# Optimization experiments

Hardware: AMD Instinct MI355X
Metric: run time of the kernel (lower is better)

The kernel has to match this reference:

```python
import jax, jax.numpy as jnp
import numpy as np

B, S, D = 2, 1024, 512
G, H, QKD, VD = 8, 8, 64, 64
FFOUT = D

def setup_inputs() -> dict:
    key = jax.random.key(0)
    ks = jax.random.split(key, 7)
    def lin(kw, fan_in, fan_out):
        lim = 1.0 / np.sqrt(fan_in)
        kw1, kw2 = jax.random.split(kw)
        w = jax.random.uniform(kw1, (fan_in, fan_out), jnp.float32, -lim, lim)
        b = jax.random.uniform(kw2, (fan_out,), jnp.float32, -lim, lim)
        return w, b
    x = jax.random.normal(ks[0], (B, S, D), jnp.float32)
    Wq_w, Wq_b = lin(ks[1], D, H * G * QKD)
    Wkv_w, Wkv_b = lin(ks[2], D, G * (QKD + VD))
    Wz_w, Wz_b = lin(ks[3], VD * H * G, FFOUT)
    return {"x": x, "Wq_w": Wq_w, "Wq_b": Wq_b, "Wkv_w": Wkv_w,
            "Wkv_b": Wkv_b, "Wz_w": Wz_w, "Wz_b": Wz_b}

def reference(x, Wq_w, Wq_b, Wkv_w, Wkv_b, Wz_w, Wz_b):
    # m defaults to x (cross-attention path of GQA with m=None)
    m = x
    scale = 1.0 / np.sqrt(QKD)
    q = (x @ Wq_w + Wq_b).reshape(B, S, G, H, QKD)          # [b,s,g,h,d]
    kv = m @ Wkv_w + Wkv_b                                   # [b,S,g*(qk+v)]
    k = kv[..., : G * QKD].reshape(B, S, G, QKD)             # [b,S,g,d]
    v = kv[..., G * QKD :].reshape(B, S, G, VD)              # [b,S,g,d]
    qk = jnp.einsum('bsghd,bSgd->bghsS', q, k)               # [b,g,h,s,S]
    # attdropout=0 -> Identity; softmax applied to scaled scores
    weight = jax.nn.softmax(qk * scale, axis=-1)
    z = jnp.einsum('bghsS,bSgd->bsghd', weight, v)           # [b,s,g,h,d]
    z = z.reshape(B, S, G * H * VD)
    out = jax.nn.leaky_relu(z @ Wz_w + Wz_b, negative_slope=0.01)
    return out
```

## Files before the change

kernel.cpp:

```cpp
#include <hip/hip_runtime.h>
#include <stdint.h>

#define B_   2
#define S_   1024
#define D_   512
#define G_   8
#define H_   8
#define QKD_ 64
#define VD_  64
#define T_   (B_ * S_)
#define QC_  (G_ * H_ * QKD_)
#define KVC_ (G_ * (QKD_ + VD_))
#define SPLITK_ 4

typedef __attribute__((ext_vector_type(8))) short short8;
typedef __attribute__((ext_vector_type(4))) float f32x4;

#if __has_builtin(__builtin_amdgcn_exp2f)
#define EXP2(x) __builtin_amdgcn_exp2f(x)
#else
#define EXP2(x) exp2f(x)
#endif

__device__ __forceinline__ unsigned short f2bf(float f) {
    unsigned u = __builtin_bit_cast(unsigned, f);
    u += 0x7FFF + ((u >> 16) & 1);
    return (unsigned short)(u >> 16);
}

__device__ __forceinline__ unsigned pk2(float lo, float hi) {
    return (unsigned)f2bf(lo) | ((unsigned)f2bf(hi) << 16);
}

__global__ __launch_bounds__(256) void f32_to_bf16_vec(
    const float* __restrict__ in, unsigned short* __restrict__ out, int n4)
{
    int i = blockIdx.x * 256 + threadIdx.x;
    if (i >= n4) return;
    float4 v = ((const float4*)in)[i];
    ushort4 o;
    o.x = f2bf(v.x); o.y = f2bf(v.y); o.z = f2bf(v.z); o.w = f2bf(v.w);
    ((ushort4*)out)[i] = o;
}

__global__ __launch_bounds__(256) void transpose_f32_bf16(
    const float* __restrict__ in, unsigned short* __restrict__ out, int K, int N)
{
    __shared__ float tile[32][33];
    int n0 = blockIdx.x * 32, k0 = blockIdx.y * 32;
    int tx = threadIdx.x & 31, ty = threadIdx.x >> 5;
    #pragma unroll
    for (int i = 0; i < 4; i++)
        tile[ty + i * 8][tx] = in[(size_t)(k0 + ty + i * 8) * N + n0 + tx];
    __syncthreads();
    #pragma unroll
    for (int i = 0; i < 4; i++)
        out[(size_t)(n0 + ty + i * 8) * K + k0 + tx] = f2bf(tile[tx][ty + i * 8]);
}

template <int OUT_MODE>
__global__ __launch_bounds__(256) void gemm_bt(
    const unsigned short* __restrict__ A,
    const unsigned short* __restrict__ Bt,
    const float* __restrict__ bias,
    const float* __restrict__ bias2,
    void* __restrict__ Cout,
    unsigned short* __restrict__ Kbo,
    unsigned short* __restrict__ Vto,
    int M, int N, int Kst, int Klen)
{
    constexpr int BM = 128, BN = 128, BK = 32, LDT = 40;
    __shared__ __attribute__((aligned(16))) unsigned short As[BM * LDT];
    __shared__ __attribute__((aligned(16))) unsigned short Bs[BN * LDT];
    const int tid = threadIdx.x;
    const int m0 = blockIdx.y * BM, n0 = blockIdx.x * BN;
    const int kz = blockIdx.z;
    const int koff = kz * Klen;
    const int lane = tid & 63, w = tid >> 6;
    const int wm = w >> 1, wn = w & 1;
    const int cl = lane & 15, gr = lane >> 4;

    f32x4 acc[4][4];
    #pragma unroll
    for (int i = 0; i < 4; i++)
        #pragma unroll
        for (int j = 0; j < 4; j++) acc[i][j] = {0.f, 0.f, 0.f, 0.f};

    const int o0 = tid * 16;
    const int row0 = o0 >> 6, ce0 = (o0 & 63) >> 1;
    const int o1 = o0 + 4096;
    const int row1 = o1 >> 6, ce1 = (o1 & 63) >> 1;

    const int nkt = Klen / BK;
    for (int kt = 0; kt < nkt; kt++) {
        const int k0 = koff + kt * BK;
        int4 a0 = *(const int4*)(A + (size_t)(m0 + row0) * Kst + k0 + ce0);
        int4 a1 = *(const int4*)(A + (size_t)(m0 + row1) * Kst + k0 + ce1);
        int4 b0 = *(const int4*)(Bt + (size_t)(n0 + row0) * Kst + k0 + ce0);
        int4 b1 = *(const int4*)(Bt + (size_t)(n0 + row1) * Kst + k0 + ce1);
        __syncthreads();
        *(int4*)&As[row0 * LDT + ce0] = a0;
        *(int4*)&As[row1 * LDT + ce1] = a1;
        *(int4*)&Bs[row0 * LDT + ce0] = b0;
        *(int4*)&Bs[row1 * LDT + ce1] = b1;
        __syncthreads();
        short8 af[4], bfr[4];
        #pragma unroll
        for (int mr = 0; mr < 4; mr++)
            af[mr] = *(const short8*)&As[(wm * 64 + mr * 16 + cl) * LDT + gr * 8];
        #pragma unroll
        for (int nr = 0; nr < 4; nr++)
            bfr[nr] = *(const short8*)&Bs[(wn * 64 + nr * 16 + cl) * LDT + gr * 8];
        #pragma unroll
        for (int mr = 0; mr < 4; mr++)
            #pragma unroll
            for (int nr = 0; nr < 4; nr++)
                acc[mr][nr] = __builtin_amdgcn_mfma_f32_16x16x32_bf16(
                    af[mr], bfr[nr], acc[mr][nr], 0, 0, 0);
    }

    #pragma unroll
    for (int mr = 0; mr < 4; mr++) {
        #pragma unroll
        for (int nr = 0; nr < 4; nr++) {
            const int col = n0 + wn * 64 + nr * 16 + cl;
            float bv = 0.f;
            if (OUT_MODE == 3)
                bv = (col < QC_) ? bias[col] : bias2[col - QC_];
            #pragma unroll
            for (int j = 0; j < 4; j++) {
                const int row = m0 + wm * 64 + mr * 16 + gr * 4 + j;
                float v = acc[mr][nr][j] + bv;
                if (OUT_MODE == 2) {
                    ((float*)Cout)[(size_t)kz * M * N + (size_t)row * N + col] = v;
                } else {
                    const unsigned short h = f2bf(v);
                    if (col < QC_) {
                        ((unsigned short*)Cout)[(size_t)row * QC_ + col] = h;
                    } else {
                        const int c2 = col - QC_;
                        const int bb = row >> 10, s = row & 1023;
                        if (c2 < G_ * QKD_) {
                            const int g = c2 >> 6, d = c2 & 63;
                            Kbo[((size_t)((bb << 3) + g) * 1024 + s) * 64 + d] = h;
                        } else {
                            const int c3 = c2 - G_ * QKD_;
                            const int g = c3 >> 6, d = c3 & 63;
                            Vto[((size_t)((bb << 3) + g) * 64 + d) * 1024 + s] = h;
                        }
                    }
                }
            }
        }
    }
}

__global__ __launch_bounds__(256) void reduce_splitk(
    const float* __restrict__ part, const float* __restrict__ bias,
    float* __restrict__ out, int n4)
{
    int i = blockIdx.x * 256 + threadIdx.x;
    if (i >= n4) return;
    const float4* p = (const float4*)part;
    float4 s = p[i];
    #pragma unroll
    for (int k = 1; k < SPLITK_; k++) {
        float4 t = p[(size_t)k * n4 + i];
        s.x += t.x; s.y += t.y; s.z += t.z; s.w += t.w;
    }
    float4 bv = ((const float4*)bias)[i & (D_ / 4 - 1)];
    s.x += bv.x; s.y += bv.y; s.z += bv.z; s.w += bv.w;
    s.x = s.x > 0.f ? s.x : 0.01f * s.x;
    s.y = s.y > 0.f ? s.y : 0.01f * s.y;
    s.z = s.z > 0.f ? s.z : 0.01f * s.z;
    s.w = s.w > 0.f ? s.w : 0.01f * s.w;
    ((float4*)out)[i] = s;
}

__global__ __launch_bounds__(512) void attn_kernel(
    const unsigned short* __restrict__ Qb,
    const unsigned short* __restrict__ Kb,
    const unsigned short* __restrict__ Vtb,
    unsigned short* __restrict__ Zb)
{
    __shared__ __attribute__((aligned(16))) unsigned short KT[2][64 * 64];
    __shared__ __attribute__((aligned(16))) unsigned short VT[2][64 * 64];

    const int tid = threadIdx.x;
    const int w = tid >> 6, lane = tid & 63;
    const int cl = lane & 15, gr = (lane >> 4) & 3;
    const int bid = blockIdx.x;
    const int qt = bid & 7, head = bid >> 3;
    const int b = head >> 6, gh = head & 63;
    const int g = gh >> 3;
    const int qrow0 = qt * 128 + w * 16;

    const unsigned short* Qp =
        Qb + (size_t)(b * S_ + qrow0 + cl) * QC_ + gh * 64 + gr * 8;
    const short8 q0 = *(const short8*)(Qp);
    const short8 q1 = *(const short8*)(Qp + 32);

    const unsigned short* Khead = Kb + (size_t)(b * G_ + g) * (S_ * 64);
    const unsigned short* Vhead = Vtb + (size_t)(b * G_ + g) * (64 * S_);

    const int kr = tid >> 3, kc = (tid & 7) * 16;
    const int kw = kr * 128 + (kc ^ ((kr & 7) << 4));
    const int vd = tid >> 3, vg = tid & 7;
    const int vbase = (vg & 3) * 4 + (vg >> 2) * 32;
    const int vw = vd * 128 + ((vg * 16) ^ ((vd & 7) << 4));

    char* const kt0 = (char*)&KT[0][0];
    char* const kt1 = (char*)&KT[1][0];
    char* const vt0 = (char*)&VT[0][0];
    char* const vt1 = (char*)&VT[1][0];

    const int sw = (cl & 7) << 4;
    const int cA = (gr * 16) ^ sw;
    const int cB = (64 + gr * 16) ^ sw;

    const float C = 0.18033688011112042f;
    float l = 0.f;
    f32x4 acc[4];
    #pragma unroll
    for (int d = 0; d < 4; d++) acc[d] = {0.f, 0.f, 0.f, 0.f};

    int4 skA;
    uint2 sv0, sv1;

#define LOADS(key0_)                                                          \
    {                                                                         \
        const int _k0 = (key0_);                                              \
        skA = *(const int4*)(Khead + (size_t)(_k0 + kr) * 64 + (kc >> 1));    \
        const unsigned short* _vr = Vhead + (size_t)vd * S_ + _k0 + vbase;    \
        sv0 = *(const uint2*)(_vr);                                           \
        sv1 = *(const uint2*)(_vr + 16);                                      \
    }
#define WRITES(kt_, vt_)                                                      \
    {                                                                         \
        *(int4*)((kt_) + kw) = skA;                                           \
        *(int4*)((vt_) + vw) =                                                \
            make_int4((int)sv0.x, (int)sv0.y, (int)sv1.x, (int)sv1.y);        \
    }

    LOADS(0);
    WRITES(kt0, vt0);

    for (int kt = 0; kt < S_ / 64; kt++) {
        const int sel = kt & 1;
        __syncthreads();
        if (kt + 1 < S_ / 64) LOADS((kt + 1) * 64);

        const char* kbuf = sel ? kt1 : kt0;
        const char* vbuf = sel ? vt1 : vt0;

        f32x4 s[4];
        #pragma unroll
        for (int bb = 0; bb < 4; bb++) {
            const char* kr_ = kbuf + (bb * 16 + cl) * 128;
            short8 kf0 = *(const short8*)(kr_ + cA);
            short8 kf1 = *(const short8*)(kr_ + cB);
            f32x4 z = {0.f, 0.f, 0.f, 0.f};
            z = __builtin_amdgcn_mfma_f32_16x16x32_bf16(kf0, q0, z, 0, 0, 0);
            z = __builtin_amdgcn_mfma_f32_16x16x32_bf16(kf1, q1, z, 0, 0, 0);
            s[bb] = z;
        }

        float p[4][4];
        #pragma unroll
        for (int bb = 0; bb < 4; bb++)
            #pragma unroll
            for (int j = 0; j < 4; j++)
                p[bb][j] = EXP2(s[bb][j] * C);

        float a0 = (p[0][0] + p[0][1]) + (p[0][2] + p[0][3]);
        float a1 = (p[1][0] + p[1][1]) + (p[1][2] + p[1][3]);
        float a2 = (p[2][0] + p[2][1]) + (p[2][2] + p[2][3]);
        float a3 = (p[3][0] + p[3][1]) + (p[3][2] + p[3][3]);
        l += (a0 + a1) + (a2 + a3);

        union { unsigned u[4]; short8 v; } pb0, pb1;
        asm("v_cvt_pk_bf16_f32 %0, %1, %2" : "=v"(pb0.u[0]) : "v"(p[0][0]), "v"(p[0][1]));
        asm("v_cvt_pk_bf16_f32 %0, %1, %2" : "=v"(pb0.u[1]) : "v"(p[0][2]), "v"(p[0][3]));
        asm("v_cvt_pk_bf16_f32 %0, %1, %2" : "=v"(pb0.u[2]) : "v"(p[1][0]), "v"(p[1][1]));
        asm("v_cvt_pk_bf16_f32 %0, %1, %2" : "=v"(pb0.u[3]) : "v"(p[1][2]), "v"(p[1][3]));
        asm("v_cvt_pk_bf16_f32 %0, %1, %2" : "=v"(pb1.u[0]) : "v"(p[2][0]), "v"(p[2][1]));
        asm("v_cvt_pk_bf16_f32 %0, %1, %2" : "=v"(pb1.u[1]) : "v"(p[2][2]), "v"(p[2][3]));
        asm("v_cvt_pk_bf16_f32 %0, %1, %2" : "=v"(pb1.u[2]) : "v"(p[3][0]), "v"(p[3][1]));
        asm("v_cvt_pk_bf16_f32 %0, %1, %2" : "=v"(pb1.u[3]) : "v"(p[3][2]), "v"(p[3][3]));

        #pragma unroll
        for (int db = 0; db < 4; db++) {
            const char* vr = vbuf + (db * 16 + cl) * 128;
            short8 vf0 = *(const short8*)(vr + cA);
            short8 vf1 = *(const short8*)(vr + cB);
            acc[db] = __builtin_amdgcn_mfma_f32_16x16x32_bf16(vf0, pb0.v, acc[db], 0, 0, 0);
            acc[db] = __builtin_amdgcn_mfma_f32_16x16x32_bf16(vf1, pb1.v, acc[db], 0, 0, 0);
        }

        if (kt + 1 < S_ / 64) {
            if (sel) { WRITES(kt0, vt0); } else { WRITES(kt1, vt1); }
        }
    }
#undef LOADS
#undef WRITES

    l += __shfl_xor(l, 16);
    l += __shfl_xor(l, 32);
    const float rl = 1.0f / l;
    unsigned short* zrow = Zb + (size_t)(b * S_ + qrow0 + cl) * QC_ + gh * 64;
    #pragma unroll
    for (int db = 0; db < 4; db++) {
        uint2 o;
        o.x = pk2(acc[db][0] * rl, acc[db][1] * rl);
        o.y = pk2(acc[db][2] * rl, acc[db][3] * rl);
        *(uint2*)(zrow + db * 16 + gr * 4) = o;
    }
}

extern "C" void kernel_launch(void* const* d_in, const int* in_sizes, int n_in,
                              void* d_out, int out_size, void* d_ws, size_t ws_size,
                              hipStream_t stream)
{
    const float* x     = (const float*)d_in[0];
    const float* Wq_w  = (const float*)d_in[1];
    const float* Wq_b  = (const float*)d_in[2];
    const float* Wkv_w = (const float*)d_in[3];
    const float* Wkv_b = (const float*)d_in[4];
    const float* Wz_w  = (const float*)d_in[5];
    const float* Wz_b  = (const float*)d_in[6];
    float* out = (float*)d_out;

    unsigned short* ws   = (unsigned short*)d_ws;
    unsigned short* xb   = ws;
    unsigned short* WqT  = xb   + (size_t)T_ * D_;
    unsigned short* WkvT = WqT  + (size_t)QC_ * D_;
    unsigned short* WzT  = WkvT + (size_t)KVC_ * D_;
    unsigned short* Qb   = WzT  + (size_t)D_ * QC_;
    unsigned short* Kb   = Qb   + (size_t)T_ * QC_;
    unsigned short* Vtb  = Kb   + (size_t)B_ * G_ * S_ * 64;
    unsigned short* Zb   = Vtb  + (size_t)B_ * G_ * 64 * S_;
    float* Pp = (float*)Qb;

    f32_to_bf16_vec<<<(T_ * D_ / 4 + 255) / 256, 256, 0, stream>>>(x, xb, T_ * D_ / 4);
    transpose_f32_bf16<<<dim3(QC_ / 32, D_ / 32), 256, 0, stream>>>(Wq_w, WqT, D_, QC_);
    transpose_f32_bf16<<<dim3(KVC_ / 32, D_ / 32), 256, 0, stream>>>(Wkv_w, WkvT, D_, KVC_);
    transpose_f32_bf16<<<dim3(D_ / 32, QC_ / 32), 256, 0, stream>>>(Wz_w, WzT, QC_, D_);

    gemm_bt<3><<<dim3((QC_ + KVC_) / 128, T_ / 128), 256, 0, stream>>>(
        xb, WqT, Wq_b, Wkv_b, Qb, Kb, Vtb, T_, QC_ + KVC_, D_, D_);

    attn_kernel<<<B_ * G_ * H_ * (S_ / 128), 512, 0, stream>>>(Qb, Kb, Vtb, Zb);

    gemm_bt<2><<<dim3(D_ / 128, T_ / 128, SPLITK_), 256, 0, stream>>>(
        Zb, WzT, nullptr, nullptr, Pp, nullptr, nullptr, T_, D_, QC_, QC_ / SPLITK_);
    reduce_splitk<<<(T_ * D_ / 4 + 255) / 256, 256, 0, stream>>>(
        Pp, Wz_b, out, T_ * D_ / 4);
}
```

Baseline: 189.8 us.

## Use direct global-to-LDS loads with XOR swizzle and BK=64 in GEMM

```diff
diff --git a/kernel.cpp b/kernel.cpp
--- a/kernel.cpp
+++ b/kernel.cpp
@@ -32,6 +32,12 @@
     return (unsigned)f2bf(lo) | ((unsigned)f2bf(hi) << 16);
 }
 
+__device__ __forceinline__ void gload16(const unsigned short* g, void* l) {
+    __builtin_amdgcn_global_load_lds(
+        (const __attribute__((address_space(1))) void*)g,
+        (__attribute__((address_space(3))) void*)l, 16, 0, 0);
+}
+
 __global__ __launch_bounds__(256) void f32_to_bf16_vec(
     const float* __restrict__ in, unsigned short* __restrict__ out, int n4)
 {
@@ -69,9 +75,9 @@
     unsigned short* __restrict__ Vto,
     int M, int N, int Kst, int Klen)
 {
-    constexpr int BM = 128, BN = 128, BK = 32, LDT = 40;
-    __shared__ __attribute__((aligned(16))) unsigned short As[BM * LDT];
-    __shared__ __attribute__((aligned(16))) unsigned short Bs[BN * LDT];
+    constexpr int BM = 128, BN = 128, BK = 64;
+    __shared__ __attribute__((aligned(16))) unsigned short As[BM * BK];
+    __shared__ __attribute__((aligned(16))) unsigned short Bs[BN * BK];
     const int tid = threadIdx.x;
     const int m0 = blockIdx.y * BM, n0 = blockIdx.x * BN;
     const int kz = blockIdx.z;
@@ -80,43 +86,53 @@
     const int wm = w >> 1, wn = w & 1;
     const int cl = lane & 15, gr = lane >> 4;
 
+    const int rowc = tid >> 3;
+    const int gcol = ((((tid & 7) * 16) ^ ((rowc & 7) << 4)) >> 1);
+    char* const asb = (char*)As;
+    char* const bsb = (char*)Bs;
+    const int wbase = w * 1024;
+
     f32x4 acc[4][4];
     #pragma unroll
     for (int i = 0; i < 4; i++)
         #pragma unroll
         for (int j = 0; j < 4; j++) acc[i][j] = {0.f, 0.f, 0.f, 0.f};
 
-    const int o0 = tid * 16;
-    const int row0 = o0 >> 6, ce0 = (o0 & 63) >> 1;
-    const int o1 = o0 + 4096;
-    const int row1 = o1 >> 6, ce1 = (o1 & 63) >> 1;
-
+    const int sw = (cl & 7) << 4;
     const int nkt = Klen / BK;
     for (int kt = 0; kt < nkt; kt++) {
         const int k0 = koff + kt * BK;
-        int4 a0 = *(const int4*)(A + (size_t)(m0 + row0) * Kst + k0 + ce0);
-        int4 a1 = *(const int4*)(A + (size_t)(m0 + row1) * Kst + k0 + ce1);
-        int4 b0 = *(const int4*)(Bt + (size_t)(n0 + row0) * Kst + k0 + ce0);
-        int4 b1 = *(const int4*)(Bt + (size_t)(n0 + row1) * Kst + k0 + ce1);
         __syncthreads();
-        *(int4*)&As[row0 * LDT + ce0] = a0;
-        *(int4*)&As[row1 * LDT + ce1] = a1;
-        *(int4*)&Bs[row0 * LDT + ce0] = b0;
-        *(int4*)&Bs[row1 * LDT + ce1] = b1;
+        #pragma unroll
+        for (int c = 0; c < 4; c++) {
+            gload16(A  + (size_t)(m0 + c * 32 + rowc) * Kst + k0 + gcol,
+                    asb + c * 4096 + wbase);
+            gload16(Bt + (size_t)(n0 + c * 32 + rowc) * Kst + k0 + gcol,
+                    bsb + c * 4096 + wbase);
+        }
         __syncthreads();
-        short8 af[4], bfr[4];
-        #pragma unroll
-        for (int mr = 0; mr < 4; mr++)
-            af[mr] = *(const short8*)&As[(wm * 64 + mr * 16 + cl) * LDT + gr * 8];
-        #pragma unroll
-        for (int nr = 0; nr < 4; nr++)
-            bfr[nr] = *(const short8*)&Bs[(wn * 64 + nr * 16 + cl) * LDT + gr * 8];
+        short8 a0[4], a1[4], b0[4], b1[4];
+        #pragma unroll
+        for (int mr = 0; mr < 4; mr++) {
+            const char* ar = asb + (wm * 64 + mr * 16 + cl) * 128;
+            a0[mr] = *(const short8*)(ar + ((gr * 16) ^ sw));
+            a1[mr] = *(const short8*)(ar + ((64 + gr * 16) ^ sw));
+        }
+        #pragma unroll
+        for (int nr = 0; nr < 4; nr++) {
+            const char* br = bsb + (wn * 64 + nr * 16 + cl) * 128;
+            b0[nr] = *(const short8*)(br + ((gr * 16) ^ sw));
+            b1[nr] = *(const short8*)(br + ((64 + gr * 16) ^ sw));
+        }
         #pragma unroll
         for (int mr = 0; mr < 4; mr++)
             #pragma unroll
-            for (int nr = 0; nr < 4; nr++)
+            for (int nr = 0; nr < 4; nr++) {
                 acc[mr][nr] = __builtin_amdgcn_mfma_f32_16x16x32_bf16(
-                    af[mr], bfr[nr], acc[mr][nr], 0, 0, 0);
+                    a0[mr], b0[nr], acc[mr][nr], 0, 0, 0);
+                acc[mr][nr] = __builtin_amdgcn_mfma_f32_16x16x32_bf16(
+                    a1[mr], b1[nr], acc[mr][nr], 0, 0, 0);
+            }
     }
 
     #pragma unroll
```

Result: no change. 186.5 us (-1.7%).
